# Optimization experiments

Hardware: AMD Instinct MI355X
Metric: run time of the kernel (lower is better)

Reference implementation:

```python
import jax, jax.numpy as jnp
import numpy as np

B, S, D = 4, 2048, 768
H, DH = 12, 64  # num heads, head dim


def setup_inputs() -> dict:
    key = jax.random.key(0)
    ks = jax.random.split(key, 4)
    scale = 0.02
    return {
        "hidden_states": jax.random.normal(ks[0], (B, S, D), dtype=jnp.float32),
        "attention_mask": jnp.zeros((B, 1, 1, S), dtype=jnp.float32),
        "Wq": jax.random.normal(ks[1], (D, D), dtype=jnp.float32) * scale,
        "bq": jnp.zeros((D,), dtype=jnp.float32),
        "Wk": jax.random.normal(ks[2], (D, D), dtype=jnp.float32) * scale,
        "bk": jnp.zeros((D,), dtype=jnp.float32),
        "Wv": jax.random.normal(ks[3], (D, D), dtype=jnp.float32) * scale,
        "bv": jnp.zeros((D,), dtype=jnp.float32),
    }


def _split_heads(x):
    # [B, S, D] -> [B, H, S, DH]
    b, s, _ = x.shape
    return x.reshape(b, s, H, DH).transpose(0, 2, 1, 3)


def reference(hidden_states, attention_mask, Wq, bq, Wk, bk, Wv, bv):
    q = _split_heads(hidden_states @ Wq.T + bq)
    k = _split_heads(hidden_states @ Wk.T + bk)
    v = _split_heads(hidden_states @ Wv.T + bv)
    # scores: [B, H, S, S]
    scores = jnp.einsum("bhqd,bhkd->bhqk", q, k) / jnp.sqrt(jnp.float32(DH))
    scores = scores + attention_mask
    probs = jax.nn.softmax(scores, axis=-1)
    # dropout prob = 0.0 (eval) -> identity
    ctx = jnp.einsum("bhqk,bhkd->bhqd", probs, v)
    ctx = ctx.transpose(0, 2, 1, 3).reshape(hidden_states.shape[0], hidden_states.shape[1], D)
    return ctx
```

## Files before the change

kernel.cpp:

```cpp
#include <hip/hip_runtime.h>

#define S_LEN 2048
#define DMODEL 768
#define NH 12
#define DHEAD 64
#define BATCH 4
#define MROWS (BATCH * S_LEN)
#define NQKV 2304

using short8 = __attribute__((ext_vector_type(8))) short;
using f32x4  = __attribute__((ext_vector_type(4))) float;
using f32x16 = __attribute__((ext_vector_type(16))) float;

typedef const __attribute__((address_space(1))) void* gas_ptr;
typedef __attribute__((address_space(3))) void* las_ptr;

__device__ __forceinline__ void gl2lds16(const void* g, void* l) {
  __builtin_amdgcn_global_load_lds((gas_ptr)(unsigned long long)g,
                                   (las_ptr)(unsigned int)(unsigned long long)l,
                                   16, 0, 0);
}

__device__ inline unsigned short f2bf(float f) {
  union { float f; unsigned int u; } c; c.f = f;
  unsigned int u = c.u;
  unsigned int r = (u + 0x7FFFu + ((u >> 16) & 1u)) >> 16;
  return (unsigned short)r;
}

__device__ inline unsigned int pack2bf(float a, float b) {
  union { float f; unsigned int u; } ca, cb;
  ca.f = a; cb.f = b;
  unsigned int ua = ca.u, ub = cb.u;
  ua = (ua + 0x7FFFu + ((ua >> 16) & 1u)) >> 16;
  ub = (ub + 0x7FFFu + ((ub >> 16) & 1u)) & 0xFFFF0000u;
  return ua | ub;
}

__global__ __launch_bounds__(256) void prep_kernel(
    const float* __restrict__ hs, const float* __restrict__ Wq,
    const float* __restrict__ Wk, const float* __restrict__ Wv,
    const float* __restrict__ mask,
    unsigned short* __restrict__ Xb, unsigned short* __restrict__ Wall,
    float* __restrict__ mask2)
{
  const int NX = MROWS * DMODEL / 4;
  const int NW = DMODEL * DMODEL / 4;
  const int NM = (BATCH * S_LEN) / 4;
  int i = blockIdx.x * 256 + threadIdx.x;
  if (i < NX) {
    float4 f = ((const float4*)hs)[i];
    ushort4 o = { f2bf(f.x), f2bf(f.y), f2bf(f.z), f2bf(f.w) };
    ((ushort4*)Xb)[i] = o;
  } else if (i < NX + 3 * NW) {
    int j = i - NX;
    int sec = j / NW, r = j - sec * NW;
    const float* src = (sec == 0) ? Wq : (sec == 1) ? Wk : Wv;
    float4 f = ((const float4*)src)[r];
    ushort4 o = { f2bf(f.x), f2bf(f.y), f2bf(f.z), f2bf(f.w) };
    ((ushort4*)(Wall + (size_t)sec * DMODEL * DMODEL))[r] = o;
  } else if (i < NX + 3 * NW + NM) {
    int r = i - NX - 3 * NW;
    float4 m = ((const float4*)mask)[r];
    float4 o = { m.x - 10.f, m.y - 10.f, m.z - 10.f, m.w - 10.f };
    ((float4*)mask2)[r] = o;
  }
}

__global__ __launch_bounds__(256) void qkv_gemm(
    const unsigned short* __restrict__ Xb,
    const unsigned short* __restrict__ Wall,
    const float* __restrict__ bq,
    const float* __restrict__ bk,
    const float* __restrict__ bv,
    unsigned short* __restrict__ Out)
{
  __shared__ __align__(16) short As[128][64];
  __shared__ __align__(16) short Bs[128][64];

  int m0 = blockIdx.y * 128;
  int n0 = blockIdx.x * 128;
  int t = threadIdx.x;
  int w = t >> 6, lane = t & 63, lg = lane >> 4, lc = lane & 15;
  int wr = (w >> 1) * 64, wc = (w & 1) * 64;

  int srow = lane >> 3;
  int schunk = (lane & 7) ^ srow;

  f32x4 acc[4][4] = {};

  for (int k0 = 0; k0 < DMODEL; k0 += 64) {
    __syncthreads();
    for (int it = 0; it < 4; ++it) {
      int rb = w * 32 + it * 8;
      int r = rb + srow;
      gl2lds16(&Xb[(size_t)(m0 + r) * DMODEL + k0 + schunk * 8], &As[rb][0]);
      gl2lds16(&Wall[(size_t)(n0 + r) * DMODEL + k0 + schunk * 8], &Bs[rb][0]);
    }
    __syncthreads();
    for (int ks = 0; ks < 2; ++ks) {
      short8 a[4], b[4];
      for (int mt = 0; mt < 4; ++mt)
        a[mt] = *(const short8*)&As[wr + mt * 16 + lc][(((ks * 4 + lg) ^ (lc & 7))) * 8];
      for (int nt = 0; nt < 4; ++nt)
        b[nt] = *(const short8*)&Bs[wc + nt * 16 + lc][(((ks * 4 + lg) ^ (lc & 7))) * 8];
      for (int mt = 0; mt < 4; ++mt)
        for (int nt = 0; nt < 4; ++nt)
          acc[mt][nt] = __builtin_amdgcn_mfma_f32_16x16x32_bf16(a[mt], b[nt], acc[mt][nt], 0, 0, 0);
    }
  }

  for (int nt = 0; nt < 4; ++nt) {
    int col = n0 + wc + nt * 16 + lc;
    float bb = (col < 768) ? bq[col] : (col < 1536) ? bk[col - 768] : bv[col - 1536];
    float sc = (col < 768) ? 0.125f : 1.0f;
    for (int mt = 0; mt < 4; ++mt) {
      int row = m0 + wr + mt * 16 + lg * 4;
      for (int i = 0; i < 4; ++i)
        Out[(size_t)(row + i) * NQKV + col] = f2bf((acc[mt][nt][i] + bb) * sc);
    }
  }
}

__global__ __launch_bounds__(256) void v_transpose(
    const unsigned short* __restrict__ QKV,
    unsigned short* __restrict__ Vt)
{
  int st = blockIdx.x, h = blockIdx.y, b = blockIdx.z;
  __shared__ __align__(16) short Ls[64][72];
  int t = threadIdx.x;
  int s0 = st * 64;
  int lr = t >> 3, ls = (t & 7) * 8;
  for (int it = 0; it < 2; ++it) {
    int r = lr + it * 32;
    *(int4*)&Ls[r][ls] =
        *(const int4*)&QKV[(size_t)(b * S_LEN + s0 + r) * NQKV + 1536 + h * DHEAD + ls];
  }
  __syncthreads();
  int d = t & 63, sq = t >> 6;
  size_t obase = ((size_t)((b * NH + h) * DHEAD + d)) * S_LEN + s0;
  for (int it = 0; it < 2; ++it) {
    int ss = sq + it * 4;
    short8 vv;
    for (int j = 0; j < 8; ++j) vv[j] = Ls[ss * 8 + j][d];
    *(short8*)&Vt[obase + ss * 8] = vv;
  }
}

__global__ __launch_bounds__(256, 4) void flash_attn(
    const unsigned short* __restrict__ QKV,
    const unsigned short* __restrict__ Vt,
    const float* __restrict__ mask2,
    float* __restrict__ out)
{
  int qt = blockIdx.x, h = blockIdx.y, b = blockIdx.z;
  __shared__ __align__(16) short Ks[64][64];
  __shared__ __align__(16) short Vts[64][64];
  __shared__ __align__(16) short Ps[4][32][68];

  int t = threadIdx.x, w = t >> 6, lane = t & 63;
  int m31 = lane & 31, hf = lane >> 5;
  int q0 = qt * 128;
  int srow = lane >> 3;
  int schunk = (lane & 7) ^ srow;

  short8 qf[4];
  {
    size_t qrow = (size_t)(b * S_LEN + q0 + w * 32 + m31) * NQKV + h * DHEAD;
    for (int kk = 0; kk < 4; ++kk)
      qf[kk] = *(const short8*)&QKV[qrow + kk * 16 + hf * 8];
  }

  float lsum = 0.f;
  f32x16 o[2] = {};
  size_t vtbase = (size_t)((b * NH + h) * DHEAD) * S_LEN;
  const float* mrow = mask2 + (size_t)b * S_LEN;

  for (int kt = 0; kt < S_LEN / 64; ++kt) {
    int k0 = kt * 64;
    __syncthreads();
    {
      size_t kbase = (size_t)(b * S_LEN + k0) * NQKV + 768 + h * DHEAD;
      for (int it = 0; it < 2; ++it) {
        int rb = w * 16 + it * 8;
        int r = rb + srow;
        gl2lds16(&QKV[kbase + (size_t)r * NQKV + schunk * 8], &Ks[rb][0]);
        gl2lds16(&Vt[vtbase + (size_t)r * S_LEN + k0 + schunk * 8], &Vts[rb][0]);
      }
    }
    __syncthreads();

    f32x16 s[2] = {};
    for (int kk = 0; kk < 4; ++kk)
      for (int mt = 0; mt < 2; ++mt) {
        int r = mt * 32 + m31;
        short8 ak = *(const short8*)&Ks[r][((kk * 2 + hf) ^ (r & 7)) * 8];
        s[mt] = __builtin_amdgcn_mfma_f32_32x32x16_bf16(ak, qf[kk], s[mt], 0, 0, 0);
      }

    for (int mt = 0; mt < 2; ++mt)
      for (int g = 0; g < 4; ++g) {
        float4 mv = *(const float4*)&mrow[k0 + mt * 32 + g * 8 + hf * 4];
        float p0 = __expf(s[mt][g * 4 + 0] + mv.x);
        float p1 = __expf(s[mt][g * 4 + 1] + mv.y);
        float p2 = __expf(s[mt][g * 4 + 2] + mv.z);
        float p3 = __expf(s[mt][g * 4 + 3] + mv.w);
        lsum += (p0 + p1) + (p2 + p3);
        uint2 d2;
        d2.x = pack2bf(p0, p1);
        d2.y = pack2bf(p2, p3);
        *(uint2*)&Ps[w][m31][mt * 32 + g * 8 + hf * 4] = d2;
      }

    __builtin_amdgcn_s_waitcnt(0);

    for (int kk = 0; kk < 4; ++kk) {
      short8 ap = *(const short8*)&Ps[w][m31][kk * 16 + hf * 8];
      for (int nt = 0; nt < 2; ++nt) {
        int r = nt * 32 + m31;
        short8 bv = *(const short8*)&Vts[r][((kk * 2 + hf) ^ (r & 7)) * 8];
        o[nt] = __builtin_amdgcn_mfma_f32_32x32x16_bf16(ap, bv, o[nt], 0, 0, 0);
      }
    }
  }

  lsum += __shfl_xor(lsum, 32, 64);
  float inv = 1.0f / lsum;
  float lv[16];
  for (int r = 0; r < 16; ++r)
    lv[r] = __shfl(inv, (r & 3) + 8 * (r >> 2) + 4 * hf, 64);

  for (int nt = 0; nt < 2; ++nt)
    for (int r = 0; r < 16; ++r) {
      int qrow = (r & 3) + 8 * (r >> 2) + 4 * hf;
      int q = q0 + w * 32 + qrow;
      out[(size_t)(b * S_LEN + q) * DMODEL + h * DHEAD + nt * 32 + m31] = o[nt][r] * lv[r];
    }
}

extern "C" void kernel_launch(void* const* d_in, const int* in_sizes, int n_in,
                              void* d_out, int out_size, void* d_ws, size_t ws_size,
                              hipStream_t stream) {
  const float* hs   = (const float*)d_in[0];
  const float* mask = (const float*)d_in[1];
  const float* Wq   = (const float*)d_in[2];
  const float* bq   = (const float*)d_in[3];
  const float* Wk   = (const float*)d_in[4];
  const float* bk   = (const float*)d_in[5];
  const float* Wv   = (const float*)d_in[6];
  const float* bv   = (const float*)d_in[7];
  float* out = (float*)d_out;

  char* ws = (char*)d_ws;
  const size_t XB_BYTES   = (size_t)MROWS * DMODEL * 2;
  const size_t QKV_BYTES  = (size_t)MROWS * NQKV * 2;
  const size_t WALL_BYTES = (size_t)NQKV * DMODEL * 2;
  unsigned short* Xb    = (unsigned short*)ws;
  unsigned short* QKV   = (unsigned short*)(ws + XB_BYTES);
  unsigned short* Wall  = (unsigned short*)(ws + XB_BYTES + QKV_BYTES);
  float*          mask2 = (float*)(ws + XB_BYTES + QKV_BYTES + WALL_BYTES);
  unsigned short* Vtg   = Xb;

  const int NX = MROWS * DMODEL / 4;
  const int NW = DMODEL * DMODEL / 4;
  const int NM = (BATCH * S_LEN) / 4;
  int nprep = NX + 3 * NW + NM;
  prep_kernel<<<(nprep + 255) / 256, 256, 0, stream>>>(hs, Wq, Wk, Wv, mask, Xb, Wall, mask2);

  qkv_gemm<<<dim3(NQKV / 128, MROWS / 128), 256, 0, stream>>>(Xb, Wall, bq, bk, bv, QKV);

  v_transpose<<<dim3(S_LEN / 64, NH, BATCH), 256, 0, stream>>>(QKV, Vtg);

  flash_attn<<<dim3(S_LEN / 128, NH, BATCH), 256, 0, stream>>>(QKV, Vtg, mask2, out);
}
```

Before: 236.2 us.

## Double-buffer K/V tiles, keep P in registers via lane shuffles, use exp2

The flash attention loop now double-buffers K and V^T tiles in LDS, prefetching the next tile right after the current tile has been loaded into registers, so the second barrier per iteration is gone. The probability matrix no longer makes a round trip through LDS; it is rearranged with cross-half-wavefront shuffles into the MFMA A-operand layout. log2(e) is folded into the Q scale and the mask so exp2f can replace __expf. Keeping the K and V fragments in registers raises register pressure, so launch bounds drop from 4 to 3 blocks per CU, which may lower occupancy.

```diff
diff --git a/kernel.cpp b/kernel.cpp
--- a/kernel.cpp
+++ b/kernel.cpp
@@ -7,6 +7,7 @@
 #define BATCH 4
 #define MROWS (BATCH * S_LEN)
 #define NQKV 2304
+#define LOG2E 1.44269504088896340736f
 
 using short8 = __attribute__((ext_vector_type(8))) short;
 using f32x4  = __attribute__((ext_vector_type(4))) float;
@@ -62,7 +63,8 @@
   } else if (i < NX + 3 * NW + NM) {
     int r = i - NX - 3 * NW;
     float4 m = ((const float4*)mask)[r];
-    float4 o = { m.x - 10.f, m.y - 10.f, m.z - 10.f, m.w - 10.f };
+    float4 o = { (m.x - 10.f) * LOG2E, (m.y - 10.f) * LOG2E,
+                 (m.z - 10.f) * LOG2E, (m.w - 10.f) * LOG2E };
     ((float4*)mask2)[r] = o;
   }
 }
@@ -113,7 +115,7 @@
   for (int nt = 0; nt < 4; ++nt) {
     int col = n0 + wc + nt * 16 + lc;
     float bb = (col < 768) ? bq[col] : (col < 1536) ? bk[col - 768] : bv[col - 1536];
-    float sc = (col < 768) ? 0.125f : 1.0f;
+    float sc = (col < 768) ? (0.125f * LOG2E) : 1.0f;
     for (int mt = 0; mt < 4; ++mt) {
       int row = m0 + wr + mt * 16 + lg * 4;
       for (int i = 0; i < 4; ++i)
@@ -147,16 +149,15 @@
   }
 }
 
-__global__ __launch_bounds__(256, 4) void flash_attn(
+__global__ __launch_bounds__(256, 3) void flash_attn(
     const unsigned short* __restrict__ QKV,
     const unsigned short* __restrict__ Vt,
     const float* __restrict__ mask2,
     float* __restrict__ out)
 {
   int qt = blockIdx.x, h = blockIdx.y, b = blockIdx.z;
-  __shared__ __align__(16) short Ks[64][64];
-  __shared__ __align__(16) short Vts[64][64];
-  __shared__ __align__(16) short Ps[4][32][68];
+  __shared__ __align__(16) short Ks[2][64][64];
+  __shared__ __align__(16) short Vts[2][64][64];
 
   int t = threadIdx.x, w = t >> 6, lane = t & 63;
   int m31 = lane & 31, hf = lane >> 5;
@@ -164,6 +165,10 @@
   int srow = lane >> 3;
   int schunk = (lane & 7) ^ srow;
 
+  size_t vtbase = (size_t)((b * NH + h) * DHEAD) * S_LEN;
+  const float* mrow = mask2 + (size_t)b * S_LEN;
+  size_t kbase0 = (size_t)(b * S_LEN) * NQKV + 768 + h * DHEAD;
+
   short8 qf[4];
   {
     size_t qrow = (size_t)(b * S_LEN + q0 + w * 32 + m31) * NQKV + h * DHEAD;
@@ -171,56 +176,72 @@
       qf[kk] = *(const short8*)&QKV[qrow + kk * 16 + hf * 8];
   }
 
+  {
+    for (int it = 0; it < 2; ++it) {
+      int rb = w * 16 + it * 8;
+      int r = rb + srow;
+      gl2lds16(&QKV[kbase0 + (size_t)r * NQKV + schunk * 8], &Ks[0][rb][0]);
+      gl2lds16(&Vt[vtbase + (size_t)r * S_LEN + schunk * 8], &Vts[0][rb][0]);
+    }
+  }
+
   float lsum = 0.f;
   f32x16 o[2] = {};
-  size_t vtbase = (size_t)((b * NH + h) * DHEAD) * S_LEN;
-  const float* mrow = mask2 + (size_t)b * S_LEN;
 
   for (int kt = 0; kt < S_LEN / 64; ++kt) {
+    int cur = kt & 1;
     int k0 = kt * 64;
     __syncthreads();
-    {
-      size_t kbase = (size_t)(b * S_LEN + k0) * NQKV + 768 + h * DHEAD;
+
+    short8 kf[8], vf[8];
+    for (int kk = 0; kk < 4; ++kk)
+      for (int mt = 0; mt < 2; ++mt) {
+        int r = mt * 32 + m31;
+        int c = ((kk * 2 + hf) ^ (r & 7)) * 8;
+        kf[kk * 2 + mt] = *(const short8*)&Ks[cur][r][c];
+        vf[kk * 2 + mt] = *(const short8*)&Vts[cur][r][c];
+      }
+
+    if (kt + 1 < S_LEN / 64) {
+      int k1 = k0 + 64;
       for (int it = 0; it < 2; ++it) {
         int rb = w * 16 + it * 8;
         int r = rb + srow;
-        gl2lds16(&QKV[kbase + (size_t)r * NQKV + schunk * 8], &Ks[rb][0]);
-        gl2lds16(&Vt[vtbase + (size_t)r * S_LEN + k0 + schunk * 8], &Vts[rb][0]);
+        gl2lds16(&QKV[kbase0 + (size_t)(k1 + r) * NQKV + schunk * 8], &Ks[cur ^ 1][rb][0]);
+        gl2lds16(&Vt[vtbase + (size_t)r * S_LEN + k1 + schunk * 8], &Vts[cur ^ 1][rb][0]);
       }
     }
-    __syncthreads();
 
     f32x16 s[2] = {};
     for (int kk = 0; kk < 4; ++kk)
-      for (int mt = 0; mt < 2; ++mt) {
-        int r = mt * 32 + m31;
-        short8 ak = *(const short8*)&Ks[r][((kk * 2 + hf) ^ (r & 7)) * 8];
-        s[mt] = __builtin_amdgcn_mfma_f32_32x32x16_bf16(ak, qf[kk], s[mt], 0, 0, 0);
-      }
-
+      for (int mt = 0; mt < 2; ++mt)
+        s[mt] = __builtin_amdgcn_mfma_f32_32x32x16_bf16(kf[kk * 2 + mt], qf[kk], s[mt], 0, 0, 0);
+
+    unsigned int pk[16], xk[16];
     for (int mt = 0; mt < 2; ++mt)
       for (int g = 0; g < 4; ++g) {
         float4 mv = *(const float4*)&mrow[k0 + mt * 32 + g * 8 + hf * 4];
-        float p0 = __expf(s[mt][g * 4 + 0] + mv.x);
-        float p1 = __expf(s[mt][g * 4 + 1] + mv.y);
-        float p2 = __expf(s[mt][g * 4 + 2] + mv.z);
-        float p3 = __expf(s[mt][g * 4 + 3] + mv.w);
+        float p0 = exp2f(s[mt][g * 4 + 0] + mv.x);
+        float p1 = exp2f(s[mt][g * 4 + 1] + mv.y);
+        float p2 = exp2f(s[mt][g * 4 + 2] + mv.z);
+        float p3 = exp2f(s[mt][g * 4 + 3] + mv.w);
         lsum += (p0 + p1) + (p2 + p3);
-        uint2 d2;
-        d2.x = pack2bf(p0, p1);
-        d2.y = pack2bf(p2, p3);
-        *(uint2*)&Ps[w][m31][mt * 32 + g * 8 + hf * 4] = d2;
+        pk[mt * 8 + g * 2 + 0] = pack2bf(p0, p1);
+        pk[mt * 8 + g * 2 + 1] = pack2bf(p2, p3);
       }
 
-    __builtin_amdgcn_s_waitcnt(0);
+    for (int i = 0; i < 16; ++i)
+      xk[i] = (unsigned int)__shfl_xor((int)pk[i], 32, 64);
 
     for (int kk = 0; kk < 4; ++kk) {
-      short8 ap = *(const short8*)&Ps[w][m31][kk * 16 + hf * 8];
-      for (int nt = 0; nt < 2; ++nt) {
-        int r = nt * 32 + m31;
-        short8 bv = *(const short8*)&Vts[r][((kk * 2 + hf) ^ (r & 7)) * 8];
-        o[nt] = __builtin_amdgcn_mfma_f32_32x32x16_bf16(ap, bv, o[nt], 0, 0, 0);
-      }
+      int base = (kk >> 1) * 8 + (kk & 1) * 4;
+      union { unsigned int u[4]; short8 s8; } af;
+      af.u[0] = hf ? xk[base + 2] : pk[base + 0];
+      af.u[1] = hf ? xk[base + 3] : pk[base + 1];
+      af.u[2] = hf ? pk[base + 2] : xk[base + 0];
+      af.u[3] = hf ? pk[base + 3] : xk[base + 1];
+      for (int nt = 0; nt < 2; ++nt)
+        o[nt] = __builtin_amdgcn_mfma_f32_32x32x16_bf16(af.s8, vf[kk * 2 + nt], o[nt], 0, 0, 0);
     }
   }
 
```

Measured after the change: 248.8 us. +5.3%, slower.
